# Kernel optimization log

Hardware: AMD Instinct MI355X
Metric: run time of the kernel (lower is better)

The kernel has to match this reference:

```python
import jax, jax.numpy as jnp
import numpy as np


def _bspline_basis(x, t, k):
    """Bottom-up Cox-de Boor recurrence (same math as the recursive torch B()).
    x: [B, C] evaluation points, t: [B, T] knots. Returns basis [B, T-k-1, C].
    """
    tt = t[:, :, None]   # [B, T, 1]
    xb = x[:, None, :]   # [B, 1, C]
    # degree-0 indicator: B0[i] = 1 if t[i] <= x < t[i+1]
    Bk = ((tt[:, :-1] <= xb) & (xb < tt[:, 1:])).astype(x.dtype)  # [B, T-1, C]
    for kk in range(1, k + 1):
        d1 = tt[:, kk:-1] - tt[:, :-(kk + 1)]   # t[i+kk]   - t[i]
        d2 = tt[:, kk + 1:] - tt[:, 1:-kk]      # t[i+kk+1] - t[i+1]
        w1 = jnp.where(d1 == 0, 0.0, (xb - tt[:, :-(kk + 1)]) / jnp.where(d1 == 0, 1.0, d1))
        w2 = jnp.where(d2 == 0, 0.0, (tt[:, kk + 1:] - xb) / jnp.where(d2 == 0, 1.0, d2))
        Bk = w1 * Bk[:, :-1] + w2 * Bk[:, 1:]   # [B, T-kk-1, C]
    return Bk


def setup_inputs() -> dict:
    key = jax.random.key(0)
    k1, k2, k3 = jax.random.split(key, 3)
    B, n, C, K = 4096, 64, 256, 3
    T = n + K + 1  # 68 knots
    coefficients = jax.random.normal(k1, (B, n, C), dtype=jnp.float32)
    # knots must be nondecreasing for a valid B-spline
    knots = jnp.sort(jax.random.uniform(k2, (B, T), dtype=jnp.float32), axis=1)
    inpce = jax.random.uniform(k3, (B, 1), dtype=jnp.float32)
    return {"coefficients": coefficients, "knots": knots, "inpce": inpce}


def reference(coefficients, knots, inpce):
    # coefficients: [B, n, C], knots: [B, T], inpce: [B, 1]; T = n + 4, cubic (k=3)
    B, n, C = coefficients.shape
    x = jnp.broadcast_to(inpce, (B, C))       # == inpce.repeat(1, C)
    basis = _bspline_basis(x, knots, 3)       # [B, n, C]
    # out = sum_i c[:, i, :] * B(x, 3, i, t)
    return jnp.einsum('bnc,bnc->bc', coefficients, basis)
```

## Files before the change

### kernel.cpp

```cpp
#include <hip/hip_runtime.h>

#define NB   64
#define NC   256
#define NT   68
#define DEG  3

__global__ __launch_bounds__(256) void bspline_kernel(
    const float* __restrict__ coeff,
    const float* __restrict__ knots,
    const float* __restrict__ x_in,
    float* __restrict__ out,
    int Btotal)
{
    const int b = blockIdx.x;
    if (b >= Btotal) return;
    const int c = threadIdx.x;

    __shared__ float t[NT];
    if (c < NT) t[c] = knots[(size_t)b * NT + c];
    __syncthreads();

    const float x = x_in[b];

    int j = -1;
    #pragma unroll
    for (int i = 0; i < NT - 1; ++i) {
        if (t[i] <= x && x < t[i + 1]) j = i;
    }

    float acc = 0.0f;
    if (j >= 0) {
        float N[DEG + 1] = {1.0f, 0.0f, 0.0f, 0.0f};
        #pragma unroll
        for (int kk = 1; kk <= DEG; ++kk) {
            #pragma unroll
            for (int m = DEG; m >= 0; --m) {
                if (m > kk) continue;
                const int i = j - kk + m;
                const float oldm1 = (m - 1 >= 0) ? N[m - 1] : 0.0f;
                const float oldm  = (m <= kk - 1) ? N[m] : 0.0f;
                auto tc = [&](int idx) {
                    idx = idx < 0 ? 0 : (idx > NT - 1 ? NT - 1 : idx);
                    return t[idx];
                };
                const float t_i   = tc(i);
                const float t_ik  = tc(i + kk);
                const float t_i1  = tc(i + 1);
                const float t_ik1 = tc(i + kk + 1);
                const float d1 = t_ik  - t_i;
                const float d2 = t_ik1 - t_i1;
                const float w1 = (d1 == 0.0f) ? 0.0f : (x - t_i)   / d1;
                const float w2 = (d2 == 0.0f) ? 0.0f : (t_ik1 - x) / d2;
                N[m] = w1 * oldm1 + w2 * oldm;
            }
        }

        const float* crow = coeff + (size_t)b * NB * NC + c;
        #pragma unroll
        for (int m = 0; m <= DEG; ++m) {
            const int i = j - DEG + m;
            if (i >= 0 && i < NB) {
                acc = fmaf(N[m], crow[(size_t)i * NC], acc);
            }
        }
    }

    out[(size_t)b * NC + c] = acc;
}

extern "C" void kernel_launch(void* const* d_in, const int* in_sizes, int n_in,
                              void* d_out, int out_size, void* d_ws, size_t ws_size,
                              hipStream_t stream) {
    const float* coeff = (const float*)d_in[0];
    const float* knots = (const float*)d_in[1];
    const float* x_in  = (const float*)d_in[2];
    float* out = (float*)d_out;

    const int B = in_sizes[2];

    bspline_kernel<<<B, NC, 0, stream>>>(coeff, knots, x_in, out, B);
}
```

Baseline: 307.8 us.

## Map one wavefront per batch row with float4 IO and ballot interval search

Each 256-thread block now handles four batch rows, one 64-lane wavefront per row, and each lane processes four channels through float4 loads and stores. The per-thread 67-step serial knot scan becomes a parallel comparison across lanes, with the first matching interval picked by ballot and find-first-set. This aims to cut redundant per-thread search work and the number of memory instructions, and to reduce block count. The basis recurrence is still computed redundantly in every lane. Where several intervals match because of repeated knots, the first match is now chosen instead of the last, which may differ from the reference on degenerate knot vectors.

Result: faster. 300.1 us (-2.5%).

```diff
diff --git a/kernel.cpp b/kernel.cpp
--- a/kernel.cpp
+++ b/kernel.cpp
@@ -4,6 +4,7 @@
 #define NC   256
 #define NT   68
 #define DEG  3
+#define BPB  4
 
 __global__ __launch_bounds__(256) void bspline_kernel(
     const float* __restrict__ coeff,
@@ -12,23 +13,35 @@
     float* __restrict__ out,
     int Btotal)
 {
-    const int b = blockIdx.x;
+    const int wave = threadIdx.x >> 6;
+    const int lane = threadIdx.x & 63;
+    const int b = blockIdx.x * BPB + wave;
+
+    __shared__ float t_s[BPB][NT];
+    if (b < Btotal) {
+        t_s[wave][lane] = knots[(size_t)b * NT + lane];
+        if (lane < NT - 64) t_s[wave][64 + lane] = knots[(size_t)b * NT + 64 + lane];
+    }
+    __syncthreads();
     if (b >= Btotal) return;
-    const int c = threadIdx.x;
 
-    __shared__ float t[NT];
-    if (c < NT) t[c] = knots[(size_t)b * NT + c];
-    __syncthreads();
-
+    const float* t = t_s[wave];
     const float x = x_in[b];
 
     int j = -1;
-    #pragma unroll
-    for (int i = 0; i < NT - 1; ++i) {
-        if (t[i] <= x && x < t[i + 1]) j = i;
+    {
+        const bool c1 = (t[lane] <= x) && (x < t[lane + 1]);
+        const unsigned long long m1 = __ballot(c1);
+        if (m1) {
+            j = __ffsll((long long)m1) - 1;
+        } else {
+            const bool c2 = (lane < NT - 1 - 64) && (t[64 + lane] <= x) && (x < t[65 + lane]);
+            const unsigned long long m2 = __ballot(c2);
+            if (m2) j = 64 + __ffsll((long long)m2) - 1;
+        }
     }
 
-    float acc = 0.0f;
+    float4 acc = make_float4(0.f, 0.f, 0.f, 0.f);
     if (j >= 0) {
         float N[DEG + 1] = {1.0f, 0.0f, 0.0f, 0.0f};
         #pragma unroll
@@ -55,17 +68,21 @@
             }
         }
 
-        const float* crow = coeff + (size_t)b * NB * NC + c;
+        const float* base = coeff + (size_t)b * NB * NC + 4 * lane;
         #pragma unroll
         for (int m = 0; m <= DEG; ++m) {
             const int i = j - DEG + m;
             if (i >= 0 && i < NB) {
-                acc = fmaf(N[m], crow[(size_t)i * NC], acc);
+                const float4 v = *(const float4*)(base + (size_t)i * NC);
+                acc.x = fmaf(N[m], v.x, acc.x);
+                acc.y = fmaf(N[m], v.y, acc.y);
+                acc.z = fmaf(N[m], v.z, acc.z);
+                acc.w = fmaf(N[m], v.w, acc.w);
             }
         }
     }
 
-    out[(size_t)b * NC + c] = acc;
+    *(float4*)(out + (size_t)b * NC + 4 * lane) = acc;
 }
 
 extern "C" void kernel_launch(void* const* d_in, const int* in_sizes, int n_in,
@@ -78,5 +95,6 @@
 
     const int B = in_sizes[2];
 
-    bspline_kernel<<<B, NC, 0, stream>>>(coeff, knots, x_in, out, B);
+    const int grid = (B + BPB - 1) / BPB;
+    bspline_kernel<<<grid, 256, 0, stream>>>(coeff, knots, x_in, out, B);
 }
```
